# Optimization experiments

Hardware: AMD Instinct MI355X
Metric: run time of the kernel (lower is better)

Reference implementation:

```python
import jax, jax.numpy as jnp
import numpy as np

EPS = 1e-6  # GLOBAL_EPS
D_QK = 192
ATTN_DIM = 768


def setup_inputs() -> dict:
    key = jax.random.key(0)
    ks = jax.random.split(key, 12)
    B, C, H, W = 16, 192, 56, 56
    d_qk, d_v = D_QK, 2 * D_QK
    attn_dim, inner = ATTN_DIM, d_v
    r = lambda k, s, sc=0.05: jax.random.normal(k, s, dtype=jnp.float32) * sc
    return {
        "x": jax.random.normal(ks[0], (B, C, H, W), dtype=jnp.float32),
        "proj_w": r(ks[1], (attn_dim, C)),          # 1x1 conv + BN folded
        "proj_b": r(ks[2], (attn_dim,)),
        "dwc_w": r(ks[3], (attn_dim, 1, 3, 3)),     # depthwise 3x3, BN folded
        "dwc_b": r(ks[4], (attn_dim,)),
        "g_w": r(ks[5], (inner, attn_dim)),          # ConvGate pointwise conv1d
        "g_b": r(ks[6], (inner,)),
        "an_w": 1.0 + r(ks[7], (inner,)),            # RMSNorm weight
        "sv": 1.0 + r(ks[8], (inner,)),              # Scale(inner, (1, inner, 1))
        "out_w": r(ks[9], (C, inner)),               # 1x1 conv + BN folded
        "out_b": r(ks[10], (C,)),
    }


def reference(x, proj_w, proj_b, dwc_w, dwc_b, g_w, g_b, an_w, sv, out_w, out_b):
    B, C, H, W = x.shape
    d_qk = D_QK
    # proj: ConvNorm 1x1 (conv + BN folded to affine)
    y = jnp.einsum("bchw,oc->bohw", x, proj_w) + proj_b[None, :, None, None]
    # dwc: RepConv depthwise 3x3 with residual (res=True)
    dw = jax.lax.conv_general_dilated(
        y, dwc_w, window_strides=(1, 1), padding="SAME",
        dimension_numbers=("NCHW", "OIHW", "NCHW"),
        feature_group_count=ATTN_DIM)
    y = dw + dwc_b[None, :, None, None] + y
    # flatten spatial -> tokens, split q/k/v along channels
    xs = y.reshape(B, ATTN_DIM, H * W)            # (B, attn_dim, N)
    q, k, v = xs[:, :d_qk], xs[:, d_qk:2 * d_qk], xs[:, 2 * d_qk:]
    # linear_attn: feature map = silu, scale = N**-0.5
    qf = jax.nn.silu(q)                            # (B, d_qk, N)
    kf = jax.nn.silu(k)
    N = H * W
    s = N ** -0.5
    # use_linear branch (N >> d): z = kT.mean(-2,True) @ q + eps ; attn = (v s)(kT s) q
    z = jnp.einsum("bd,bdn->bn", kf.mean(-1), qf)[:, None, :] + EPS  # (B, 1, N)
    vk = jnp.einsum("bvn,bdn->bvd", v * s, kf * s)  # (B, d_v, d_qk)
    attn = jnp.einsum("bvd,bdn->bvn", vk, qf) / z   # (B, d_v, N)
    # gate: pointwise conv1d on full projected features + sigmoid
    gate = jax.nn.sigmoid(jnp.einsum("bcn,oc->bon", xs, g_w) + g_b[None, :, None])
    attn = attn * gate
    # attn_norm (RMS over channels) + scale_v(v) residual
    rms = jnp.sqrt(jnp.mean(attn * attn, axis=1, keepdims=True) + EPS)
    attn = attn / rms * an_w[None, :, None] + v * sv[None, :, None]
    # out: ConvNorm 1x1 back to dim
    o = attn.reshape(B, -1, H, W)
    return jnp.einsum("bchw,oc->bohw", o, out_w) + out_b[None, :, None, None]
```

## Files before the change

kernel.cpp:

```cpp
#include <hip/hip_runtime.h>
#include <hip/hip_bf16.h>

typedef unsigned short u16;
typedef __attribute__((ext_vector_type(8))) short bf16x8;
typedef __attribute__((ext_vector_type(4))) float f32x4;

constexpr int B_ = 16, C_ = 192, H_ = 56, W_ = 56;
constexpr int N_ = H_ * W_;
constexpr int A_ = 768;
constexpr int Dq = 192;
constexpr int Vd = 384;
constexpr float EPSf = 1e-6f;

union U8 { bf16x8 v; u16 s[8]; unsigned u[4]; };

__device__ __forceinline__ float bits2f(u16 u) {
  return __uint_as_float(((unsigned)u) << 16);
}
__device__ __forceinline__ u16 f2bits(float f) {
  __hip_bfloat16 h = __float2bfloat16(f);
  u16 u;
  __builtin_memcpy(&u, &h, sizeof(u));
  return u;
}
__device__ __forceinline__ float silu_f(float v) { return v / (1.0f + __expf(-v)); }
__device__ __forceinline__ float sigm_f(float v) { return 1.0f / (1.0f + __expf(-v)); }

__device__ __forceinline__ f32x4 MFMA(bf16x8 a, bf16x8 b, f32x4 c) {
  return __builtin_amdgcn_mfma_f32_16x16x32_bf16(a, b, c, 0, 0, 0);
}

__global__ __launch_bounds__(256) void k_prep(const float* __restrict__ pw,
                                              const float* __restrict__ gw,
                                              const float* __restrict__ ow,
                                              u16* __restrict__ pwb,
                                              u16* __restrict__ gwb,
                                              u16* __restrict__ owb) {
  const int bid = blockIdx.x;
  const size_t base = ((size_t)bid * 256 + threadIdx.x) * 8;
  const float* src;
  u16* dst;
  size_t off;
  if (bid < 72) { src = pw; dst = pwb; off = base; }
  else if (bid < 216) { src = gw; dst = gwb; off = base - 147456; }
  else { src = ow; dst = owb; off = base - 442368; }
  float4 v0 = *(const float4*)&src[off];
  float4 v1 = *(const float4*)&src[off + 4];
  U8 r;
  r.s[0] = f2bits(v0.x); r.s[1] = f2bits(v0.y); r.s[2] = f2bits(v0.z); r.s[3] = f2bits(v0.w);
  r.s[4] = f2bits(v1.x); r.s[5] = f2bits(v1.y); r.s[6] = f2bits(v1.z); r.s[7] = f2bits(v1.w);
  *(bf16x8*)&dst[off] = r.v;
}

__global__ __launch_bounds__(256) void k_proj(const float* __restrict__ x,
                                              const u16* __restrict__ pwb,
                                              const float* __restrict__ pb,
                                              u16* __restrict__ y0t) {
  const int n0 = blockIdx.x * 64;
  const int oy = blockIdx.y;
  const int b = blockIdx.z;
  __shared__ u16 Xt[64][200];
  __shared__ u16 Wa[256][32];
  const int t = threadIdx.x;
  const int lane = t & 63, wid = t >> 6;
  const int fr = lane & 15, fg = lane >> 4;

  {
    const int p = t & 31, co = t >> 5;
    const float* xb = x + (size_t)b * C_ * N_ + n0 + 2 * p;
#pragma unroll
    for (int rnd = 0; rnd < 3; ++rnd) {
      const int c0 = rnd * 64 + co * 8;
      float2 v[8];
#pragma unroll
      for (int i = 0; i < 8; ++i) v[i] = *(const float2*)&xb[(size_t)(c0 + i) * N_];
      U8 r0, r1;
#pragma unroll
      for (int i = 0; i < 8; ++i) { r0.s[i] = f2bits(v[i].x); r1.s[i] = f2bits(v[i].y); }
      *(bf16x8*)&Xt[2 * p][c0] = r0.v;
      *(bf16x8*)&Xt[2 * p + 1][c0] = r1.v;
    }
  }

  f32x4 acc[4][4];
#pragma unroll
  for (int mi = 0; mi < 4; ++mi)
#pragma unroll
    for (int ni = 0; ni < 4; ++ni) acc[mi][ni] = (f32x4){0.f, 0.f, 0.f, 0.f};

  const int orow_c = t >> 2, oct_c = t & 3;
  U8 wreg[4];
#pragma unroll
  for (int jj = 0; jj < 4; ++jj)
    wreg[jj].v = *(const bf16x8*)&pwb[(size_t)(oy * 256 + orow_c + 64 * jj) * C_ + oct_c * 8];

  for (int ks = 0; ks < 6; ++ks) {
    __syncthreads();
#pragma unroll
    for (int jj = 0; jj < 4; ++jj) {
      const int orow = orow_c + 64 * jj;
      const int sw = (orow >> 1) & 3;
      *(bf16x8*)&Wa[orow][(oct_c ^ sw) * 8] = wreg[jj].v;
    }
    __syncthreads();
    if (ks < 5) {
#pragma unroll
      for (int jj = 0; jj < 4; ++jj)
        wreg[jj].v = *(const bf16x8*)&pwb[(size_t)(oy * 256 + orow_c + 64 * jj) * C_ +
                                          (ks + 1) * 32 + oct_c * 8];
    }
    bf16x8 bfrag[4];
#pragma unroll
    for (int ni = 0; ni < 4; ++ni)
      bfrag[ni] = *(const bf16x8*)&Xt[ni * 16 + fr][ks * 32 + fg * 8];
    __builtin_amdgcn_s_setprio(1);
#pragma unroll
    for (int mi = 0; mi < 4; ++mi) {
      const int ar = wid * 64 + mi * 16 + fr;
      bf16x8 a = *(const bf16x8*)&Wa[ar][(fg ^ ((ar >> 1) & 3)) * 8];
#pragma unroll
      for (int ni = 0; ni < 4; ++ni) acc[mi][ni] = MFMA(a, bfrag[ni], acc[mi][ni]);
    }
    __builtin_amdgcn_s_setprio(0);
  }
#pragma unroll
  for (int mi = 0; mi < 4; ++mi) {
    const int o4 = oy * 256 + wid * 64 + mi * 16 + fg * 4;
    const float b0 = pb[o4], b1 = pb[o4 + 1], b2 = pb[o4 + 2], b3 = pb[o4 + 3];
#pragma unroll
    for (int ni = 0; ni < 4; ++ni) {
      const int n = n0 + ni * 16 + fr;
      ushort4 pk;
      pk.x = f2bits(acc[mi][ni][0] + b0);
      pk.y = f2bits(acc[mi][ni][1] + b1);
      pk.z = f2bits(acc[mi][ni][2] + b2);
      pk.w = f2bits(acc[mi][ni][3] + b3);
      *(ushort4*)&y0t[((size_t)b * N_ + n) * A_ + o4] = pk;
    }
  }
}

__global__ __launch_bounds__(256) void k_dwc(const u16* __restrict__ y0t,
                                             const float* __restrict__ cw,
                                             const float* __restrict__ cb,
                                             u16* __restrict__ yt,
                                             u16* __restrict__ skq) {
  const int pid = blockIdx.x;
  const int L = (pid & 7) * 336 + (pid >> 3);
  const int h = L % 56, at = (L / 56) % 3, b = L / 168;
  const int t = threadIdx.x;
  const int a = at * 256 + (t & 31) * 8;
  const int wl = t >> 5;
  float w9[9][8];
  float bias[8];
#pragma unroll
  for (int j = 0; j < 8; ++j) {
    bias[j] = cb[a + j];
#pragma unroll
    for (int k = 0; k < 9; ++k) w9[k][j] = cw[(a + j) * 9 + k];
  }
  const u16* src = y0t + (size_t)b * N_ * A_ + a;
  u16* dst = yt + (size_t)b * N_ * A_ + a;
  const bool hok0 = h > 0, hok2 = h < 55;
  for (int wc = 0; wc < 7; ++wc) {
    const int w = wc * 8 + wl;
    const bool wok0 = w > 0, wok2 = w < 55;
    U8 nb[9];
#pragma unroll
    for (int dh = -1; dh <= 1; ++dh) {
      const bool hok = (dh == -1) ? hok0 : ((dh == 1) ? hok2 : true);
#pragma unroll
      for (int dw = -1; dw <= 1; ++dw) {
        const int k = (dh + 1) * 3 + (dw + 1);
        const bool ok = hok && ((dw == -1) ? wok0 : ((dw == 1) ? wok2 : true));
        if (ok)
          nb[k].v = *(const bf16x8*)&src[(size_t)((h + dh) * 56 + (w + dw)) * A_];
        else
          nb[k].u[0] = nb[k].u[1] = nb[k].u[2] = nb[k].u[3] = 0u;
      }
    }
    U8 o;
    float sv[8];
#pragma unroll
    for (int j = 0; j < 8; ++j) {
      float s = bias[j] + bits2f(nb[4].s[j]);
#pragma unroll
      for (int k = 0; k < 9; ++k) s = fmaf(w9[k][j], bits2f(nb[k].s[j]), s);
      sv[j] = s;
      o.s[j] = f2bits(s);
    }
    *(bf16x8*)&dst[(size_t)(h * 56 + w) * A_] = o.v;
    if (a < 384) {
      U8 q;
#pragma unroll
      for (int j = 0; j < 8; ++j) q.s[j] = f2bits(silu_f(sv[j]));
      *(bf16x8*)&skq[((size_t)b * N_ + h * 56 + w) * 384 + a] = q.v;
    }
  }
}

__global__ __launch_bounds__(256) void k_kfmean(const u16* __restrict__ skq,
                                                float* __restrict__ kfp) {
  const int ns = blockIdx.x, dc = blockIdx.y, b = blockIdx.z;
  const int t = threadIdx.x;
  const int dq = t & 15, nw = t >> 4;
  const u16* p = skq + ((size_t)b * N_ + ns * 448 + nw) * 384 + 192 + dc * 64 + dq * 4;
  float s0 = 0, s1 = 0, s2 = 0, s3 = 0;
#pragma unroll 4
  for (int i = 0; i < 28; ++i) {
    ushort4 u = *(const ushort4*)&p[(size_t)i * 16 * 384];
    s0 += bits2f(u.x);
    s1 += bits2f(u.y);
    s2 += bits2f(u.z);
    s3 += bits2f(u.w);
  }
  __shared__ float red[16][65];
  red[nw][dq * 4 + 0] = s0;
  red[nw][dq * 4 + 1] = s1;
  red[nw][dq * 4 + 2] = s2;
  red[nw][dq * 4 + 3] = s3;
  __syncthreads();
  if (t < 64) {
    float s = 0;
#pragma unroll
    for (int i = 0; i < 16; ++i) s += red[i][t];
    kfp[((size_t)ns * B_ + b) * Dq + dc * 64 + t] = s * (1.0f / (float)N_);
  }
}

__global__ __launch_bounds__(256) void k_z(const u16* __restrict__ skq,
                                           const float* __restrict__ kfp,
                                           float* __restrict__ zinv) {
  const int b = blockIdx.y;
  const int n = blockIdx.x * 256 + threadIdx.x;
  __shared__ float kf[192];
  if (threadIdx.x < 192) {
    float s = 0;
#pragma unroll
    for (int ns = 0; ns < 7; ++ns) s += kfp[((size_t)ns * B_ + b) * Dq + threadIdx.x];
    kf[threadIdx.x] = s;
  }
  __syncthreads();
  if (n < N_) {
    const u16* p = skq + ((size_t)b * N_ + n) * 384;
    float z = 0;
#pragma unroll
    for (int j = 0; j < 24; ++j) {
      U8 u;
      u.v = *(const bf16x8*)&p[j * 8];
#pragma unroll
      for (int i = 0; i < 8; ++i) z = fmaf(kf[j * 8 + i], bits2f(u.s[i]), z);
    }
    zinv[(size_t)b * N_ + n] = 1.0f / (z + EPSf);
  }
}

__global__ __launch_bounds__(256) void k_vk(const u16* __restrict__ skq,
                                            const u16* __restrict__ yt,
                                            float* __restrict__ vkpart) {
  const int pid = blockIdx.x;
  const int L = (pid & 7) * 42 + (pid >> 3);
  const int ns = L % 7;
  const int vblk = (L / 7) % 3;
  const int b = L / 21;
  const int t = threadIdx.x;
  const int lane = t & 63, wid = t >> 6;
  const int fr = lane & 15, fg = lane >> 4;
  const int vbase = (wid >> 1) * 64, dbase = (wid & 1) * 96;

  __shared__ u16 T[320 * 64];
  unsigned* T32 = (unsigned*)T;

  const int oct0 = t & 7;
  const int pair = (t >> 3) & 31;
  const int nb0 = ns * 448;

  U8 pre[5][2];
  auto load_pre = [&](int n0) {
    const int n = nb0 + n0 + pair * 2;
#pragma unroll
    for (int j = 0; j < 5; ++j) {
      const int oct = oct0 + 8 * j;
      const u16* srcp;
      size_t stride;
      if (j < 3) {
        srcp = skq + ((size_t)b * N_ + n) * 384 + 192 + oct * 8;
        stride = 384;
      } else {
        srcp = yt + ((size_t)b * N_ + n) * A_ + 384 + vblk * 128 + (oct - 24) * 8;
        stride = A_;
      }
      pre[j][0].v = *(const bf16x8*)srcp;
      pre[j][1].v = *(const bf16x8*)(srcp + stride);
    }
  };

  f32x4 acc[4][6];
#pragma unroll
  for (int mi = 0; mi < 4; ++mi)
#pragma unroll
    for (int ni = 0; ni < 6; ++ni) acc[mi][ni] = (f32x4){0.f, 0.f, 0.f, 0.f};

  load_pre(0);
  for (int s = 0; s < 7; ++s) {
    __syncthreads();
#pragma unroll
    for (int j = 0; j < 5; ++j) {
      const int rowb = (oct0 + 8 * j) * 8;
#pragma unroll
      for (int i = 0; i < 8; ++i) {
        const int row = rowb + i;
        const int sw = (row & 7) ^ ((row >> 3) & 7);
        const unsigned val =
            ((unsigned)pre[j][0].s[i] & 0xffffu) | (((unsigned)pre[j][1].s[i]) << 16);
        T32[row * 32 + (pair ^ (sw << 2))] = val;
      }
    }
    __syncthreads();
    if (s < 6) load_pre((s + 1) * 64);
    __builtin_amdgcn_s_setprio(1);
#pragma unroll
    for (int kf2 = 0; kf2 < 2; ++kf2) {
      bf16x8 bfrag[6];
#pragma unroll
      for (int ni = 0; ni < 6; ++ni) {
        const int row = dbase + ni * 16 + fr;
        const int sw = (row & 7) ^ ((row >> 3) & 7);
        bfrag[ni] = *(const bf16x8*)&T[row * 64 + ((kf2 * 32 + fg * 8) ^ (sw << 3))];
      }
#pragma unroll
      for (int mi = 0; mi < 4; ++mi) {
        const int row = 192 + vbase + mi * 16 + fr;
        const int sw = (row & 7) ^ ((row >> 3) & 7);
        bf16x8 a = *(const bf16x8*)&T[row * 64 + ((kf2 * 32 + fg * 8) ^ (sw << 3))];
#pragma unroll
        for (int ni = 0; ni < 6; ++ni) acc[mi][ni] = MFMA(a, bfrag[ni], acc[mi][ni]);
      }
    }
    __builtin_amdgcn_s_setprio(0);
  }
  float* base = vkpart + (((size_t)ns * 16 + b) * 3 + vblk) * (128 * 192);
#pragma unroll
  for (int mi = 0; mi < 4; ++mi)
#pragma unroll
    for (int ni = 0; ni < 6; ++ni) {
      const int v = vbase + mi * 16 + fg * 4;
      const int d = dbase + ni * 16 + fr;
      float* o = base + (size_t)v * 192 + d;
      o[0] = acc[mi][ni][0];
      o[192] = acc[mi][ni][1];
      o[384] = acc[mi][ni][2];
      o[576] = acc[mi][ni][3];
    }
}

__global__ __launch_bounds__(256) void k_vkred(const float* __restrict__ vkpart,
                                               u16* __restrict__ vkb) {
  const size_t e = ((size_t)blockIdx.x * 256 + threadIdx.x) * 8;
  constexpr size_t NSSTRIDE = (size_t)16 * 3 * 128 * 192;
  float4 s0 = {0, 0, 0, 0}, s1 = {0, 0, 0, 0};
#pragma unroll
  for (int ns = 0; ns < 7; ++ns) {
    float4 a0 = *(const float4*)&vkpart[ns * NSSTRIDE + e];
    float4 a1 = *(const float4*)&vkpart[ns * NSSTRIDE + e + 4];
    s0.x += a0.x; s0.y += a0.y; s0.z += a0.z; s0.w += a0.w;
    s1.x += a1.x; s1.y += a1.y; s1.z += a1.z; s1.w += a1.w;
  }
  const float sc = 1.0f / (float)N_;
  U8 r;
  r.s[0] = f2bits(s0.x * sc); r.s[1] = f2bits(s0.y * sc);
  r.s[2] = f2bits(s0.z * sc); r.s[3] = f2bits(s0.w * sc);
  r.s[4] = f2bits(s1.x * sc); r.s[5] = f2bits(s1.y * sc);
  r.s[6] = f2bits(s1.z * sc); r.s[7] = f2bits(s1.w * sc);
  *(bf16x8*)&vkb[e] = r.v;
}

__global__ __launch_bounds__(256) void k_gateattn(const u16* __restrict__ yt,
                                                  const u16* __restrict__ skq,
                                                  const float* __restrict__ zinv,
                                                  const u16* __restrict__ vkb,
                                                  const u16* __restrict__ gwb,
                                                  const float* __restrict__ gb,
                                                  u16* __restrict__ attnt) {
  const int pid = blockIdx.x;
  const int L = (pid & 7) * 196 + (pid >> 3);
  const int vh = L & 1;
  const int n0 = ((L >> 1) % 49) * 64;
  const int b = L / 98;
  const int t = threadIdx.x;
  const int lane = t & 63, wid = t >> 6, wm = wid >> 1, wn = wid & 1;
  const int fr = lane & 15, fg = lane >> 4;
  __shared__ u16 Wa[192][104];
  __shared__ u16 Xt[64][104];
  __shared__ float zl[64];
  if (t < 64) zl[t] = zinv[(size_t)b * N_ + n0 + t];
  const u16* yb = yt + ((size_t)b * N_ + n0) * A_;
  const u16* qb = skq + ((size_t)b * N_ + n0) * 384;
  const u16* wb0 = vkb + ((size_t)b * Vd + vh * 192) * 192;
  const u16* wb1 = gwb + (size_t)(vh * 192) * A_;

  int wrow[9], woc[9];
#pragma unroll
  for (int j = 0; j < 9; ++j) { const int idx = j * 256 + t; wrow[j] = idx / 12; woc[j] = idx % 12; }
  int xrow[3], xoc[3];
#pragma unroll
  for (int j = 0; j < 3; ++j) { const int idx = j * 256 + t; xrow[j] = idx / 12; xoc[j] = idx % 12; }

  U8 wreg[9], xreg[3];
  auto loadW = [&](int ph, int ks0) {
#pragma unroll
    for (int j = 0; j < 9; ++j) {
      const u16* s = ph ? (wb1 + (size_t)wrow[j] * A_ + ks0 + woc[j] * 8)
                        : (wb0 + (size_t)wrow[j] * 192 + ks0 + woc[j] * 8);
      wreg[j].v = *(const bf16x8*)s;
    }
  };
  auto loadX = [&](int ph, int ks0) {
#pragma unroll
    for (int j = 0; j < 3; ++j) {
      const u16* s = ph ? (yb + (size_t)xrow[j] * A_ + ks0 + xoc[j] * 8)
                        : (qb + (size_t)xrow[j] * 384 + ks0 + xoc[j] * 8);
      xreg[j].v = *(const bf16x8*)s;
    }
  };

  f32x4 acc[6][2];
#pragma unroll
  for (int mi = 0; mi < 6; ++mi)
#pragma unroll
    for (int ni = 0; ni < 2; ++ni) acc[mi][ni] = (f32x4){0.f, 0.f, 0.f, 0.f};
  uint2 pp[6][2];

  loadW(0, 0);
  loadX(0, 0);
  for (int it = 0; it < 10; ++it) {
    __syncthreads();
#pragma unroll
    for (int j = 0; j < 9; ++j) *(bf16x8*)&Wa[wrow[j]][woc[j] * 8] = wreg[j].v;
#pragma unroll
    for (int j = 0; j < 3; ++j) *(bf16x8*)&Xt[xrow[j]][xoc[j] * 8] = xreg[j].v;
    __syncthreads();
    if (it < 9) {
      const int nit = it + 1;
      const int ph = nit >= 2;
      const int ks0 = ph ? (nit - 2) * 96 : nit * 96;
      loadW(ph, ks0);
      loadX(ph, ks0);
    }
    __builtin_amdgcn_s_setprio(1);
#pragma unroll
    for (int kf = 0; kf < 3; ++kf) {
      bf16x8 bfr[2];
#pragma unroll
      for (int ni = 0; ni < 2; ++ni)
        bfr[ni] = *(const bf16x8*)&Xt[wn * 32 + ni * 16 + fr][kf * 32 + fg * 8];
#pragma unroll
      for (int mi = 0; mi < 6; ++mi) {
        bf16x8 a = *(const bf16x8*)&Wa[wm * 96 + mi * 16 + fr][kf * 32 + fg * 8];
        acc[mi][0] = MFMA(a, bfr[0], acc[mi][0]);
        acc[mi][1] = MFMA(a, bfr[1], acc[mi][1]);
      }
    }
    __builtin_amdgcn_s_setprio(0);
    if (it == 1) {
#pragma unroll
      for (int mi = 0; mi < 6; ++mi)
#pragma unroll
        for (int ni = 0; ni < 2; ++ni) {
          const float z = zl[wn * 32 + ni * 16 + fr];
          unsigned a0 = ((unsigned)f2bits(acc[mi][ni][0] * z) & 0xffffu) |
                        (((unsigned)f2bits(acc[mi][ni][1] * z) & 0xffffu) << 16);
          unsigned a1 = ((unsigned)f2bits(acc[mi][ni][2] * z) & 0xffffu) |
                        (((unsigned)f2bits(acc[mi][ni][3] * z) & 0xffffu) << 16);
          pp[mi][ni] = make_uint2(a0, a1);
          acc[mi][ni] = (f32x4){0.f, 0.f, 0.f, 0.f};
        }
    }
  }

#pragma unroll
  for (int mi = 0; mi < 6; ++mi) {
    const int vb = vh * 192 + wm * 96 + mi * 16 + fg * 4;
    const float g0 = gb[vb], g1 = gb[vb + 1], g2 = gb[vb + 2], g3 = gb[vb + 3];
#pragma unroll
    for (int ni = 0; ni < 2; ++ni) {
      const int n = n0 + wn * 32 + ni * 16 + fr;
      const uint2 p = pp[mi][ni];
      const float pv0 = bits2f((u16)(p.x & 0xffffu)), pv1 = bits2f((u16)(p.x >> 16));
      const float pv2 = bits2f((u16)(p.y & 0xffffu)), pv3 = bits2f((u16)(p.y >> 16));
      ushort4 o;
      o.x = f2bits(pv0 * sigm_f(acc[mi][ni][0] + g0));
      o.y = f2bits(pv1 * sigm_f(acc[mi][ni][1] + g1));
      o.z = f2bits(pv2 * sigm_f(acc[mi][ni][2] + g2));
      o.w = f2bits(pv3 * sigm_f(acc[mi][ni][3] + g3));
      *(ushort4*)&attnt[((size_t)b * N_ + n) * Vd + vb] = o;
    }
  }
}

__global__ __launch_bounds__(256) void k_rmsfinal(const u16* __restrict__ yt,
                                                  const float* __restrict__ anw,
                                                  const float* __restrict__ svw,
                                                  u16* __restrict__ attnt) {
  const int b = blockIdx.y;
  const int n0 = blockIdx.x * 32;
  const int t = threadIdx.x;
  __shared__ float anws[384], svws[384];
  for (int i = t; i < 384; i += 256) {
    anws[i] = anw[i];
    svws[i] = svw[i];
  }
  __syncthreads();
  const int n = n0 + (t >> 3);
  const int vs = (t & 7) * 8;
  u16* ap = attnt + ((size_t)b * N_ + n) * Vd;
  U8 av[6];
  float ss = 0.f;
#pragma unroll
  for (int j = 0; j < 6; ++j) {
    av[j].v = *(const bf16x8*)&ap[vs + j * 64];
#pragma unroll
    for (int i = 0; i < 8; ++i) {
      const float f = bits2f(av[j].s[i]);
      ss = fmaf(f, f, ss);
    }
  }
  ss += __shfl_xor(ss, 1);
  ss += __shfl_xor(ss, 2);
  ss += __shfl_xor(ss, 4);
  const float rinv = rsqrtf(ss * (1.0f / (float)Vd) + EPSf);
  const u16* vp = yt + ((size_t)b * N_ + n) * A_ + 2 * Dq;
#pragma unroll
  for (int j = 0; j < 6; ++j) {
    U8 vv, o;
    vv.v = *(const bf16x8*)&vp[vs + j * 64];
#pragma unroll
    for (int i = 0; i < 8; ++i) {
      const int v = vs + j * 64 + i;
      const float val = bits2f(av[j].s[i]) * rinv * anws[v] + bits2f(vv.s[i]) * svws[v];
      o.s[i] = f2bits(val);
    }
    *(bf16x8*)&ap[vs + j * 64] = o.v;
  }
}

__global__ __launch_bounds__(256) void k_out(const u16* __restrict__ attnt,
                                             const u16* __restrict__ owb,
                                             const float* __restrict__ ob,
                                             float* __restrict__ out) {
  const int n0 = blockIdx.x * 64;
  const int b = blockIdx.y;
  __shared__ u16 Wa[192][104];
  __shared__ u16 Xt[64][104];
  const int t = threadIdx.x;
  const int lane = t & 63, wid = t >> 6, wm = wid >> 1, wn = wid & 1;
  const int fr = lane & 15, fg = lane >> 4;
  const u16* xb = attnt + ((size_t)b * N_ + n0) * Vd;

  int wrow[9], woc[9];
#pragma unroll
  for (int j = 0; j < 9; ++j) { const int idx = j * 256 + t; wrow[j] = idx / 12; woc[j] = idx % 12; }
  int xrow[3], xoc[3];
#pragma unroll
  for (int j = 0; j < 3; ++j) { const int idx = j * 256 + t; xrow[j] = idx / 12; xoc[j] = idx % 12; }

  U8 wreg[9], xreg[3];
  auto loadW = [&](int ks0) {
#pragma unroll
    for (int j = 0; j < 9; ++j)
      wreg[j].v = *(const bf16x8*)&owb[(size_t)wrow[j] * Vd + ks0 + woc[j] * 8];
  };
  auto loadX = [&](int ks0) {
#pragma unroll
    for (int j = 0; j < 3; ++j)
      xreg[j].v = *(const bf16x8*)&xb[(size_t)xrow[j] * Vd + ks0 + xoc[j] * 8];
  };

  f32x4 acc[6][2];
#pragma unroll
  for (int mi = 0; mi < 6; ++mi)
#pragma unroll
    for (int ni = 0; ni < 2; ++ni) acc[mi][ni] = (f32x4){0.f, 0.f, 0.f, 0.f};

  loadW(0);
  loadX(0);
  for (int it = 0; it < 4; ++it) {
    __syncthreads();
#pragma unroll
    for (int j = 0; j < 9; ++j) *(bf16x8*)&Wa[wrow[j]][woc[j] * 8] = wreg[j].v;
#pragma unroll
    for (int j = 0; j < 3; ++j) *(bf16x8*)&Xt[xrow[j]][xoc[j] * 8] = xreg[j].v;
    __syncthreads();
    if (it < 3) {
      loadW((it + 1) * 96);
      loadX((it + 1) * 96);
    }
    __builtin_amdgcn_s_setprio(1);
#pragma unroll
    for (int kf = 0; kf < 3; ++kf) {
      bf16x8 bfr[2];
#pragma unroll
      for (int ni = 0; ni < 2; ++ni)
        bfr[ni] = *(const bf16x8*)&Xt[wn * 32 + ni * 16 + fr][kf * 32 + fg * 8];
#pragma unroll
      for (int mi = 0; mi < 6; ++mi) {
        bf16x8 a = *(const bf16x8*)&Wa[wm * 96 + mi * 16 + fr][kf * 32 + fg * 8];
        acc[mi][0] = MFMA(a, bfr[0], acc[mi][0]);
        acc[mi][1] = MFMA(a, bfr[1], acc[mi][1]);
      }
    }
    __builtin_amdgcn_s_setprio(0);
  }
#pragma unroll
  for (int mi = 0; mi < 6; ++mi) {
    const int c = wm * 96 + mi * 16 + fg * 4;
    const float b0 = ob[c], b1 = ob[c + 1], b2 = ob[c + 2], b3 = ob[c + 3];
#pragma unroll
    for (int ni = 0; ni < 2; ++ni) {
      const int n = n0 + wn * 32 + ni * 16 + fr;
      float* o = out + ((size_t)b * C_ + c) * N_ + n;
      o[0 * N_] = acc[mi][ni][0] + b0;
      o[1 * N_] = acc[mi][ni][1] + b1;
      o[2 * N_] = acc[mi][ni][2] + b2;
      o[3 * N_] = acc[mi][ni][3] + b3;
    }
  }
}

extern "C" void kernel_launch(void* const* d_in, const int* in_sizes, int n_in,
                              void* d_out, int out_size, void* d_ws, size_t ws_size,
                              hipStream_t stream) {
  (void)in_sizes; (void)n_in; (void)out_size; (void)ws_size;
  const float* x = (const float*)d_in[0];
  const float* pw = (const float*)d_in[1];
  const float* pb = (const float*)d_in[2];
  const float* cw = (const float*)d_in[3];
  const float* cb = (const float*)d_in[4];
  const float* gw = (const float*)d_in[5];
  const float* gb = (const float*)d_in[6];
  const float* anw = (const float*)d_in[7];
  const float* svw = (const float*)d_in[8];
  const float* ow = (const float*)d_in[9];
  const float* ob = (const float*)d_in[10];
  float* out = (float*)d_out;

  char* ws = (char*)d_ws;
  const size_t szY = (size_t)B_ * N_ * A_ * 2;
  u16* y0t = (u16*)(ws);
  u16* attnt = (u16*)(ws);
  float* vkpart = (float*)(ws + 38535168);
  u16* vkb = (u16*)(ws + 71565312);
  u16* yt = (u16*)(ws + szY);
  u16* skq = (u16*)(ws + 2 * szY);
  char* ws2 = ws + 2 * szY + 38535168;
  float* kfp = (float*)(ws2);
  float* zinv = (float*)(ws2 + 86016);
  u16* pwb = (u16*)(ws2 + 86016 + 200704);
  u16* gwb = (u16*)(ws2 + 86016 + 200704 + 294912);
  u16* owb = (u16*)(ws2 + 86016 + 200704 + 294912 + 589824);

  k_prep<<<dim3(252), 256, 0, stream>>>(pw, gw, ow, pwb, gwb, owb);
  k_proj<<<dim3(49, 3, 16), 256, 0, stream>>>(x, pwb, pb, y0t);
  k_dwc<<<dim3(2688), 256, 0, stream>>>(y0t, cw, cb, yt, skq);
  k_kfmean<<<dim3(7, 3, 16), 256, 0, stream>>>(skq, kfp);
  k_z<<<dim3(13, 16), 256, 0, stream>>>(skq, kfp, zinv);
  k_vk<<<dim3(336), 256, 0, stream>>>(skq, yt, vkpart);
  k_vkred<<<dim3(576), 256, 0, stream>>>(vkpart, vkb);
  k_gateattn<<<dim3(1568), 256, 0, stream>>>(yt, skq, zinv, vkb, gwb, gb, attnt);
  k_rmsfinal<<<dim3(98, 16), 256, 0, stream>>>(yt, anw, svw, attnt);
  k_out<<<dim3(49, 16), 256, 0, stream>>>(attnt, owb, ob, out);
}
```

Measured before the change: 272.6 us.

## Drop silu buffer, recompute silu on the fly, fuse RMS into out GEMM

Removes the separate skq buffer that held silu(q,k). Silu is now recomputed from yt inside kfmean, z, vk and gateattn, which saves a large intermediate write and its re-reads. The RMS-norm and residual kernel is folded into k_out, which holds the whole 384-wide attention tile in shared memory. Both GEMMs now load weight fragments straight from global or L2 instead of staging them through LDS, and launch bounds are tightened. The cost is repeated silu arithmetic, strided reads of yt, and weight reads that may hit L2 less efficiently.

```diff
diff --git a/kernel.cpp b/kernel.cpp
--- a/kernel.cpp
+++ b/kernel.cpp
@@ -143,8 +143,7 @@
 __global__ __launch_bounds__(256) void k_dwc(const u16* __restrict__ y0t,
                                              const float* __restrict__ cw,
                                              const float* __restrict__ cb,
-                                             u16* __restrict__ yt,
-                                             u16* __restrict__ skq) {
+                                             u16* __restrict__ yt) {
   const int pid = blockIdx.x;
   const int L = (pid & 7) * 336 + (pid >> 3);
   const int h = L % 56, at = (L / 56) % 3, b = L / 168;
@@ -180,39 +179,31 @@
       }
     }
     U8 o;
-    float sv[8];
 #pragma unroll
     for (int j = 0; j < 8; ++j) {
       float s = bias[j] + bits2f(nb[4].s[j]);
 #pragma unroll
       for (int k = 0; k < 9; ++k) s = fmaf(w9[k][j], bits2f(nb[k].s[j]), s);
-      sv[j] = s;
       o.s[j] = f2bits(s);
     }
     *(bf16x8*)&dst[(size_t)(h * 56 + w) * A_] = o.v;
-    if (a < 384) {
-      U8 q;
-#pragma unroll
-      for (int j = 0; j < 8; ++j) q.s[j] = f2bits(silu_f(sv[j]));
-      *(bf16x8*)&skq[((size_t)b * N_ + h * 56 + w) * 384 + a] = q.v;
-    }
-  }
-}
-
-__global__ __launch_bounds__(256) void k_kfmean(const u16* __restrict__ skq,
+  }
+}
+
+__global__ __launch_bounds__(256) void k_kfmean(const u16* __restrict__ yt,
                                                 float* __restrict__ kfp) {
   const int ns = blockIdx.x, dc = blockIdx.y, b = blockIdx.z;
   const int t = threadIdx.x;
   const int dq = t & 15, nw = t >> 4;
-  const u16* p = skq + ((size_t)b * N_ + ns * 448 + nw) * 384 + 192 + dc * 64 + dq * 4;
+  const u16* p = yt + ((size_t)b * N_ + ns * 448 + nw) * A_ + 192 + dc * 64 + dq * 4;
   float s0 = 0, s1 = 0, s2 = 0, s3 = 0;
 #pragma unroll 4
   for (int i = 0; i < 28; ++i) {
-    ushort4 u = *(const ushort4*)&p[(size_t)i * 16 * 384];
-    s0 += bits2f(u.x);
-    s1 += bits2f(u.y);
-    s2 += bits2f(u.z);
-    s3 += bits2f(u.w);
+    ushort4 u = *(const ushort4*)&p[(size_t)i * 16 * A_];
+    s0 += silu_f(bits2f(u.x));
+    s1 += silu_f(bits2f(u.y));
+    s2 += silu_f(bits2f(u.z));
+    s3 += silu_f(bits2f(u.w));
   }
   __shared__ float red[16][65];
   red[nw][dq * 4 + 0] = s0;
@@ -228,7 +219,7 @@
   }
 }
 
-__global__ __launch_bounds__(256) void k_z(const u16* __restrict__ skq,
+__global__ __launch_bounds__(256) void k_z(const u16* __restrict__ yt,
                                            const float* __restrict__ kfp,
                                            float* __restrict__ zinv) {
   const int b = blockIdx.y;
@@ -242,21 +233,20 @@
   }
   __syncthreads();
   if (n < N_) {
-    const u16* p = skq + ((size_t)b * N_ + n) * 384;
+    const u16* p = yt + ((size_t)b * N_ + n) * A_;
     float z = 0;
 #pragma unroll
     for (int j = 0; j < 24; ++j) {
       U8 u;
       u.v = *(const bf16x8*)&p[j * 8];
 #pragma unroll
-      for (int i = 0; i < 8; ++i) z = fmaf(kf[j * 8 + i], bits2f(u.s[i]), z);
+      for (int i = 0; i < 8; ++i) z = fmaf(kf[j * 8 + i], silu_f(bits2f(u.s[i])), z);
     }
     zinv[(size_t)b * N_ + n] = 1.0f / (z + EPSf);
   }
 }
 
-__global__ __launch_bounds__(256) void k_vk(const u16* __restrict__ skq,
-                                            const u16* __restrict__ yt,
+__global__ __launch_bounds__(256) void k_vk(const u16* __restrict__ yt,
                                             float* __restrict__ vkpart) {
   const int pid = blockIdx.x;
   const int L = (pid & 7) * 42 + (pid >> 3);
@@ -282,16 +272,12 @@
     for (int j = 0; j < 5; ++j) {
       const int oct = oct0 + 8 * j;
       const u16* srcp;
-      size_t stride;
-      if (j < 3) {
-        srcp = skq + ((size_t)b * N_ + n) * 384 + 192 + oct * 8;
-        stride = 384;
-      } else {
+      if (j < 3)
+        srcp = yt + ((size_t)b * N_ + n) * A_ + 192 + oct * 8;
+      else
         srcp = yt + ((size_t)b * N_ + n) * A_ + 384 + vblk * 128 + (oct - 24) * 8;
-        stride = A_;
-      }
       pre[j][0].v = *(const bf16x8*)srcp;
-      pre[j][1].v = *(const bf16x8*)(srcp + stride);
+      pre[j][1].v = *(const bf16x8*)(srcp + A_);
     }
   };
 
@@ -311,8 +297,12 @@
       for (int i = 0; i < 8; ++i) {
         const int row = rowb + i;
         const int sw = (row & 7) ^ ((row >> 3) & 7);
-        const unsigned val =
-            ((unsigned)pre[j][0].s[i] & 0xffffu) | (((unsigned)pre[j][1].s[i]) << 16);
+        u16 a0 = pre[j][0].s[i], a1 = pre[j][1].s[i];
+        if (j < 3) {
+          a0 = f2bits(silu_f(bits2f(a0)));
+          a1 = f2bits(silu_f(bits2f(a1)));
+        }
+        const unsigned val = ((unsigned)a0 & 0xffffu) | (((unsigned)a1) << 16);
         T32[row * 32 + (pair ^ (sw << 2))] = val;
       }
     }
@@ -375,13 +365,12 @@
   *(bf16x8*)&vkb[e] = r.v;
 }
 
-__global__ __launch_bounds__(256) void k_gateattn(const u16* __restrict__ yt,
-                                                  const u16* __restrict__ skq,
-                                                  const float* __restrict__ zinv,
-                                                  const u16* __restrict__ vkb,
-                                                  const u16* __restrict__ gwb,
-                                                  const float* __restrict__ gb,
-                                                  u16* __restrict__ attnt) {
+__global__ __launch_bounds__(256, 4) void k_gateattn(const u16* __restrict__ yt,
+                                                     const float* __restrict__ zinv,
+                                                     const u16* __restrict__ vkb,
+                                                     const u16* __restrict__ gwb,
+                                                     const float* __restrict__ gb,
+                                                     u16* __restrict__ attnt) {
   const int pid = blockIdx.x;
   const int L = (pid & 7) * 196 + (pid >> 3);
   const int vh = L & 1;
@@ -390,38 +379,22 @@
   const int t = threadIdx.x;
   const int lane = t & 63, wid = t >> 6, wm = wid >> 1, wn = wid & 1;
   const int fr = lane & 15, fg = lane >> 4;
-  __shared__ u16 Wa[192][104];
   __shared__ u16 Xt[64][104];
   __shared__ float zl[64];
   if (t < 64) zl[t] = zinv[(size_t)b * N_ + n0 + t];
   const u16* yb = yt + ((size_t)b * N_ + n0) * A_;
-  const u16* qb = skq + ((size_t)b * N_ + n0) * 384;
   const u16* wb0 = vkb + ((size_t)b * Vd + vh * 192) * 192;
   const u16* wb1 = gwb + (size_t)(vh * 192) * A_;
 
-  int wrow[9], woc[9];
-#pragma unroll
-  for (int j = 0; j < 9; ++j) { const int idx = j * 256 + t; wrow[j] = idx / 12; woc[j] = idx % 12; }
   int xrow[3], xoc[3];
 #pragma unroll
   for (int j = 0; j < 3; ++j) { const int idx = j * 256 + t; xrow[j] = idx / 12; xoc[j] = idx % 12; }
 
-  U8 wreg[9], xreg[3];
-  auto loadW = [&](int ph, int ks0) {
-#pragma unroll
-    for (int j = 0; j < 9; ++j) {
-      const u16* s = ph ? (wb1 + (size_t)wrow[j] * A_ + ks0 + woc[j] * 8)
-                        : (wb0 + (size_t)wrow[j] * 192 + ks0 + woc[j] * 8);
-      wreg[j].v = *(const bf16x8*)s;
-    }
-  };
-  auto loadX = [&](int ph, int ks0) {
-#pragma unroll
-    for (int j = 0; j < 3; ++j) {
-      const u16* s = ph ? (yb + (size_t)xrow[j] * A_ + ks0 + xoc[j] * 8)
-                        : (qb + (size_t)xrow[j] * 384 + ks0 + xoc[j] * 8);
-      xreg[j].v = *(const bf16x8*)s;
-    }
+  U8 xreg[3];
+  auto loadX = [&](int ks0) {
+#pragma unroll
+    for (int j = 0; j < 3; ++j)
+      xreg[j].v = *(const bf16x8*)&yb[(size_t)xrow[j] * A_ + ks0 + xoc[j] * 8];
   };
 
   f32x4 acc[6][2];
@@ -431,34 +404,42 @@
     for (int ni = 0; ni < 2; ++ni) acc[mi][ni] = (f32x4){0.f, 0.f, 0.f, 0.f};
   uint2 pp[6][2];
 
-  loadW(0, 0);
-  loadX(0, 0);
+  loadX(0);
   for (int it = 0; it < 10; ++it) {
     __syncthreads();
-#pragma unroll
-    for (int j = 0; j < 9; ++j) *(bf16x8*)&Wa[wrow[j]][woc[j] * 8] = wreg[j].v;
-#pragma unroll
-    for (int j = 0; j < 3; ++j) *(bf16x8*)&Xt[xrow[j]][xoc[j] * 8] = xreg[j].v;
+    const bool sl = (it < 2);
+#pragma unroll
+    for (int j = 0; j < 3; ++j) {
+      U8 w = xreg[j];
+      if (sl) {
+#pragma unroll
+        for (int i = 0; i < 8; ++i) w.s[i] = f2bits(silu_f(bits2f(w.s[i])));
+      }
+      *(bf16x8*)&Xt[xrow[j]][xoc[j] * 8] = w.v;
+    }
     __syncthreads();
     if (it < 9) {
       const int nit = it + 1;
-      const int ph = nit >= 2;
-      const int ks0 = ph ? (nit - 2) * 96 : nit * 96;
-      loadW(ph, ks0);
-      loadX(ph, ks0);
-    }
+      loadX(nit < 2 ? nit * 96 : (nit - 2) * 96);
+    }
+    const u16* wsrc;
+    size_t wstr;
+    if (it < 2) { wsrc = wb0 + it * 96; wstr = 192; }
+    else { wsrc = wb1 + (it - 2) * 96; wstr = A_; }
+    const u16* wlane = wsrc + (size_t)(wm * 96 + fr) * wstr + fg * 8;
     __builtin_amdgcn_s_setprio(1);
 #pragma unroll
     for (int kf = 0; kf < 3; ++kf) {
-      bf16x8 bfr[2];
-#pragma unroll
-      for (int ni = 0; ni < 2; ++ni)
-        bfr[ni] = *(const bf16x8*)&Xt[wn * 32 + ni * 16 + fr][kf * 32 + fg * 8];
+      U8 af[6];
+#pragma unroll
+      for (int mi = 0; mi < 6; ++mi)
+        af[mi].v = *(const bf16x8*)&wlane[(size_t)(mi * 16) * wstr + kf * 32];
+      bf16x8 bfr0 = *(const bf16x8*)&Xt[wn * 32 + fr][kf * 32 + fg * 8];
+      bf16x8 bfr1 = *(const bf16x8*)&Xt[wn * 32 + 16 + fr][kf * 32 + fg * 8];
 #pragma unroll
       for (int mi = 0; mi < 6; ++mi) {
-        bf16x8 a = *(const bf16x8*)&Wa[wm * 96 + mi * 16 + fr][kf * 32 + fg * 8];
-        acc[mi][0] = MFMA(a, bfr[0], acc[mi][0]);
-        acc[mi][1] = MFMA(a, bfr[1], acc[mi][1]);
+        acc[mi][0] = MFMA(af[mi].v, bfr0, acc[mi][0]);
+        acc[mi][1] = MFMA(af[mi].v, bfr1, acc[mi][1]);
       }
     }
     __builtin_amdgcn_s_setprio(0);
@@ -498,119 +479,91 @@
   }
 }
 
-__global__ __launch_bounds__(256) void k_rmsfinal(const u16* __restrict__ yt,
-                                                  const float* __restrict__ anw,
-                                                  const float* __restrict__ svw,
-                                                  u16* __restrict__ attnt) {
+__global__ __launch_bounds__(256, 2) void k_out(const u16* __restrict__ attnt,
+                                                const u16* __restrict__ yt,
+                                                const u16* __restrict__ owb,
+                                                const float* __restrict__ ob,
+                                                const float* __restrict__ anw,
+                                                const float* __restrict__ svw,
+                                                float* __restrict__ out) {
+  const int n0 = blockIdx.x * 64;
   const int b = blockIdx.y;
-  const int n0 = blockIdx.x * 32;
+  __shared__ u16 Xt[64][392];
+  __shared__ float anws[384], svws[384];
+  __shared__ float red[64][5];
+  __shared__ float rinv[64];
   const int t = threadIdx.x;
-  __shared__ float anws[384], svws[384];
+  const int lane = t & 63, wid = t >> 6, wm = wid >> 1, wn = wid & 1;
+  const int fr = lane & 15, fg = lane >> 4;
   for (int i = t; i < 384; i += 256) {
     anws[i] = anw[i];
     svws[i] = svw[i];
   }
+  const int srow = t >> 2, soc0 = t & 3;
+  const u16* ab = attnt + ((size_t)b * N_ + n0 + srow) * Vd;
+#pragma unroll
+  for (int j = 0; j < 12; ++j)
+    *(bf16x8*)&Xt[srow][(soc0 + 4 * j) * 8] = *(const bf16x8*)&ab[(soc0 + 4 * j) * 8];
   __syncthreads();
-  const int n = n0 + (t >> 3);
-  const int vs = (t & 7) * 8;
-  u16* ap = attnt + ((size_t)b * N_ + n) * Vd;
-  U8 av[6];
-  float ss = 0.f;
-#pragma unroll
-  for (int j = 0; j < 6; ++j) {
-    av[j].v = *(const bf16x8*)&ap[vs + j * 64];
-#pragma unroll
-    for (int i = 0; i < 8; ++i) {
-      const float f = bits2f(av[j].s[i]);
-      ss = fmaf(f, f, ss);
-    }
-  }
-  ss += __shfl_xor(ss, 1);
-  ss += __shfl_xor(ss, 2);
-  ss += __shfl_xor(ss, 4);
-  const float rinv = rsqrtf(ss * (1.0f / (float)Vd) + EPSf);
-  const u16* vp = yt + ((size_t)b * N_ + n) * A_ + 2 * Dq;
-#pragma unroll
-  for (int j = 0; j < 6; ++j) {
-    U8 vv, o;
-    vv.v = *(const bf16x8*)&vp[vs + j * 64];
-#pragma unroll
-    for (int i = 0; i < 8; ++i) {
-      const int v = vs + j * 64 + i;
-      const float val = bits2f(av[j].s[i]) * rinv * anws[v] + bits2f(vv.s[i]) * svws[v];
-      o.s[i] = f2bits(val);
-    }
-    *(bf16x8*)&ap[vs + j * 64] = o.v;
-  }
-}
-
-__global__ __launch_bounds__(256) void k_out(const u16* __restrict__ attnt,
-                                             const u16* __restrict__ owb,
-                                             const float* __restrict__ ob,
-                                             float* __restrict__ out) {
-  const int n0 = blockIdx.x * 64;
-  const int b = blockIdx.y;
-  __shared__ u16 Wa[192][104];
-  __shared__ u16 Xt[64][104];
-  const int t = threadIdx.x;
-  const int lane = t & 63, wid = t >> 6, wm = wid >> 1, wn = wid & 1;
-  const int fr = lane & 15, fg = lane >> 4;
-  const u16* xb = attnt + ((size_t)b * N_ + n0) * Vd;
-
-  int wrow[9], woc[9];
-#pragma unroll
-  for (int j = 0; j < 9; ++j) { const int idx = j * 256 + t; wrow[j] = idx / 12; woc[j] = idx % 12; }
-  int xrow[3], xoc[3];
-#pragma unroll
-  for (int j = 0; j < 3; ++j) { const int idx = j * 256 + t; xrow[j] = idx / 12; xoc[j] = idx % 12; }
-
-  U8 wreg[9], xreg[3];
-  auto loadW = [&](int ks0) {
-#pragma unroll
-    for (int j = 0; j < 9; ++j)
-      wreg[j].v = *(const bf16x8*)&owb[(size_t)wrow[j] * Vd + ks0 + woc[j] * 8];
-  };
-  auto loadX = [&](int ks0) {
-#pragma unroll
-    for (int j = 0; j < 3; ++j)
-      xreg[j].v = *(const bf16x8*)&xb[(size_t)xrow[j] * Vd + ks0 + xoc[j] * 8];
-  };
-
+  {
+    const int n = t >> 2, q = t & 3;
+    float ss = 0.f;
+#pragma unroll
+    for (int i = 0; i < 12; ++i) {
+      U8 u;
+      u.v = *(const bf16x8*)&Xt[n][q * 96 + i * 8];
+#pragma unroll
+      for (int k = 0; k < 8; ++k) {
+        const float f = bits2f(u.s[k]);
+        ss = fmaf(f, f, ss);
+      }
+    }
+    red[n][q] = ss;
+  }
+  __syncthreads();
+  if (t < 64)
+    rinv[t] = rsqrtf((red[t][0] + red[t][1] + red[t][2] + red[t][3]) * (1.0f / (float)Vd) + EPSf);
+  __syncthreads();
+  {
+    const float ri = rinv[srow];
+    const u16* vb = yt + ((size_t)b * N_ + n0 + srow) * A_ + 384;
+#pragma unroll
+    for (int j = 0; j < 12; ++j) {
+      const int oc = soc0 + 4 * j;
+      U8 xv, vv, o;
+      xv.v = *(const bf16x8*)&Xt[srow][oc * 8];
+      vv.v = *(const bf16x8*)&vb[oc * 8];
+#pragma unroll
+      for (int k = 0; k < 8; ++k) {
+        const int v = oc * 8 + k;
+        o.s[k] = f2bits(bits2f(xv.s[k]) * ri * anws[v] + bits2f(vv.s[k]) * svws[v]);
+      }
+      *(bf16x8*)&Xt[srow][oc * 8] = o.v;
+    }
+  }
+  __syncthreads();
   f32x4 acc[6][2];
 #pragma unroll
   for (int mi = 0; mi < 6; ++mi)
 #pragma unroll
     for (int ni = 0; ni < 2; ++ni) acc[mi][ni] = (f32x4){0.f, 0.f, 0.f, 0.f};
-
-  loadW(0);
-  loadX(0);
-  for (int it = 0; it < 4; ++it) {
-    __syncthreads();
-#pragma unroll
-    for (int j = 0; j < 9; ++j) *(bf16x8*)&Wa[wrow[j]][woc[j] * 8] = wreg[j].v;
-#pragma unroll
-    for (int j = 0; j < 3; ++j) *(bf16x8*)&Xt[xrow[j]][xoc[j] * 8] = xreg[j].v;
-    __syncthreads();
-    if (it < 3) {
-      loadW((it + 1) * 96);
-      loadX((it + 1) * 96);
-    }
-    __builtin_amdgcn_s_setprio(1);
-#pragma unroll
-    for (int kf = 0; kf < 3; ++kf) {
-      bf16x8 bfr[2];
-#pragma unroll
-      for (int ni = 0; ni < 2; ++ni)
-        bfr[ni] = *(const bf16x8*)&Xt[wn * 32 + ni * 16 + fr][kf * 32 + fg * 8];
-#pragma unroll
-      for (int mi = 0; mi < 6; ++mi) {
-        bf16x8 a = *(const bf16x8*)&Wa[wm * 96 + mi * 16 + fr][kf * 32 + fg * 8];
-        acc[mi][0] = MFMA(a, bfr[0], acc[mi][0]);
-        acc[mi][1] = MFMA(a, bfr[1], acc[mi][1]);
-      }
-    }
-    __builtin_amdgcn_s_setprio(0);
-  }
+  const u16* wlane = owb + (size_t)(wm * 96 + fr) * Vd + fg * 8;
+  __builtin_amdgcn_s_setprio(1);
+#pragma unroll
+  for (int kf = 0; kf < 12; ++kf) {
+    U8 af[6];
+#pragma unroll
+    for (int mi = 0; mi < 6; ++mi)
+      af[mi].v = *(const bf16x8*)&wlane[(size_t)(mi * 16) * Vd + kf * 32];
+    bf16x8 bfr0 = *(const bf16x8*)&Xt[wn * 32 + fr][kf * 32 + fg * 8];
+    bf16x8 bfr1 = *(const bf16x8*)&Xt[wn * 32 + 16 + fr][kf * 32 + fg * 8];
+#pragma unroll
+    for (int mi = 0; mi < 6; ++mi) {
+      acc[mi][0] = MFMA(af[mi].v, bfr0, acc[mi][0]);
+      acc[mi][1] = MFMA(af[mi].v, bfr1, acc[mi][1]);
+    }
+  }
+  __builtin_amdgcn_s_setprio(0);
 #pragma unroll
   for (int mi = 0; mi < 6; ++mi) {
     const int c = wm * 96 + mi * 16 + fg * 4;
@@ -651,8 +604,7 @@
   float* vkpart = (float*)(ws + 38535168);
   u16* vkb = (u16*)(ws + 71565312);
   u16* yt = (u16*)(ws + szY);
-  u16* skq = (u16*)(ws + 2 * szY);
-  char* ws2 = ws + 2 * szY + 38535168;
+  char* ws2 = ws + 2 * szY;
   float* kfp = (float*)(ws2);
   float* zinv = (float*)(ws2 + 86016);
   u16* pwb = (u16*)(ws2 + 86016 + 200704);
@@ -661,12 +613,11 @@
 
   k_prep<<<dim3(252), 256, 0, stream>>>(pw, gw, ow, pwb, gwb, owb);
   k_proj<<<dim3(49, 3, 16), 256, 0, stream>>>(x, pwb, pb, y0t);
-  k_dwc<<<dim3(2688), 256, 0, stream>>>(y0t, cw, cb, yt, skq);
-  k_kfmean<<<dim3(7, 3, 16), 256, 0, stream>>>(skq, kfp);
-  k_z<<<dim3(13, 16), 256, 0, stream>>>(skq, kfp, zinv);
-  k_vk<<<dim3(336), 256, 0, stream>>>(skq, yt, vkpart);
+  k_dwc<<<dim3(2688), 256, 0, stream>>>(y0t, cw, cb, yt);
+  k_kfmean<<<dim3(7, 3, 16), 256, 0, stream>>>(yt, kfp);
+  k_z<<<dim3(13, 16), 256, 0, stream>>>(yt, kfp, zinv);
+  k_vk<<<dim3(336), 256, 0, stream>>>(yt, vkpart);
   k_vkred<<<dim3(576), 256, 0, stream>>>(vkpart, vkb);
-  k_gateattn<<<dim3(1568), 256, 0, stream>>>(yt, skq, zinv, vkb, gwb, gb, attnt);
-  k_rmsfinal<<<dim3(98, 16), 256, 0, stream>>>(yt, anw, svw, attnt);
-  k_out<<<dim3(49, 16), 256, 0, stream>>>(attnt, owb, ob, out);
-}
+  k_gateattn<<<dim3(1568), 256, 0, stream>>>(yt, zinv, vkb, gwb, gb, attnt);
+  k_out<<<dim3(49, 16), 256, 0, stream>>>(attnt, yt, owb, ob, anw, svw, out);
+}
```

Result: slower. 381.5 us (+39.9%).
